# Kernel tuning notes

Hardware: AMD Instinct MI355X
Metric: run time of the kernel (lower is better)

## Reference

```python
import jax, jax.numpy as jnp
import numpy as np

BS, L1, L2, F_IN, HID = 32, 79, 192, 52, 128
E1, E2 = 160, 400            # intra-graph edges per drug / protein graph
SE_IN, SE_HID = L1 * L2, 2000  # 15168, 2000


def _gat(x, src, dst, W, a_s, a_d, b):
    """PyG GATConv, heads=1, add_self_loops=True, negative_slope=0.2; edge_attr ignored (edge_dim=None)."""
    n = x.shape[0]
    h = x @ W                                    # (N, HID)
    loops = jnp.arange(n, dtype=src.dtype)
    s = jnp.concatenate([src, loops])
    d = jnp.concatenate([dst, loops])
    e = jax.nn.leaky_relu((h @ a_s)[s] + (h @ a_d)[d], 0.2)   # (E+N,)
    m = jax.ops.segment_max(e, d, num_segments=n)
    w = jnp.exp(e - m[d])
    denom = jax.ops.segment_sum(w, d, num_segments=n)
    alpha = w / denom[d]                          # segment softmax over incoming edges
    return jax.ops.segment_sum(alpha[:, None] * h[s], d, num_segments=n) + b


def setup_inputs() -> dict:
    key = jax.random.key(0)
    ks = iter(jax.random.split(key, 40))
    def rn(shape, s=0.05):
        return (jax.random.normal(next(ks), shape) * s).astype(jnp.float32)
    rng = np.random.default_rng(0)
    def edges(e_per, n_per):
        off = np.arange(BS)[:, None] * n_per
        src = (rng.integers(0, n_per, (BS, e_per)) + off).reshape(-1)
        dst = (rng.integers(0, n_per, (BS, e_per)) + off).reshape(-1)
        return jnp.asarray(np.stack([src, dst]), dtype=jnp.int32)
    return {
        'x1': rn((BS * L1, F_IN), 1.0),
        'x2': rn((BS * L2, F_IN), 1.0),
        'inter': jax.random.uniform(next(ks), (BS, L1, L2), minval=0.5, maxval=1.5, dtype=jnp.float32),
        'drug_edge_index': edges(E1, L1),
        'prot_edge_index': edges(E2, L2),
        'w1': rn((F_IN, HID)), 'b1': jnp.zeros((HID,), jnp.float32),
        'w2': rn((HID, HID)), 'b2': jnp.zeros((HID,), jnp.float32),
        'gat_w': rn((6, HID, HID)), 'gat_as': rn((6, HID)),
        'gat_ad': rn((6, HID)), 'gat_b': jnp.zeros((6, HID), jnp.float32),
        'se1_w': rn((SE_IN, SE_HID)), 'se1_b': jnp.zeros((SE_HID,), jnp.float32),
        'se2_w': rn((SE_HID, SE_IN)), 'se2_b': jnp.zeros((SE_IN,), jnp.float32),
        'fc1_w': rn((256, 512)), 'fc1_b': jnp.zeros((512,), jnp.float32),
        'fc2_w': rn((512, 256)), 'fc2_b': jnp.zeros((256,), jnp.float32),
        'fc3_w': rn((256, 128)), 'fc3_b': jnp.zeros((128,), jnp.float32),
        'fc4_w': rn((128, 64)), 'fc4_b': jnp.zeros((64,), jnp.float32),
        'out_w': rn((64, 1)), 'out_b': jnp.zeros((1,), jnp.float32),
    }


def reference(x1, x2, inter, drug_edge_index, prot_edge_index,
              w1, b1, w2, b2, gat_w, gat_as, gat_ad, gat_b,
              se1_w, se1_b, se2_w, se2_b,
              fc1_w, fc1_b, fc2_w, fc2_b, fc3_w, fc3_b, fc4_w, fc4_b,
              out_w, out_b):
    relu = jax.nn.relu
    # shared node embedding MLP
    x1 = relu(relu(x1 @ w1 + b1) @ w2 + b2)
    x2 = relu(relu(x2 @ w1 + b1) @ w2 + b2)
    dsrc, ddst = drug_edge_index[0], drug_edge_index[1]
    psrc, pdst = prot_edge_index[0], prot_edge_index[1]
    # drug branch: 3 GAT layers + residual sum
    x11 = relu(_gat(x1, dsrc, ddst, gat_w[0], gat_as[0], gat_ad[0], gat_b[0]))
    x12 = relu(_gat(x11, dsrc, ddst, gat_w[1], gat_as[1], gat_ad[1], gat_b[1]))
    x13 = relu(_gat(x12, dsrc, ddst, gat_w[2], gat_as[2], gat_ad[2], gat_b[2]))
    x_l = (x11 + x12 + x13).reshape(BS, L1, HID)   # to_dense_batch (all graphs same size)
    # protein branch
    x21 = relu(_gat(x2, psrc, pdst, gat_w[3], gat_as[3], gat_ad[3], gat_b[3]))
    x22 = relu(_gat(x21, psrc, pdst, gat_w[4], gat_as[4], gat_ad[4], gat_b[4]))
    x23 = relu(_gat(x22, psrc, pdst, gat_w[5], gat_as[5], gat_ad[5], gat_b[5]))
    x_p = (x21 + x22 + x23).reshape(BS, L2, HID)
    # dense outer-product cross fusion
    inter_att = (1.0 / inter).reshape(BS, SE_IN, 1)
    x_l1 = jnp.repeat(x_l, L2, axis=1)             # (BS, L1*L2, HID)
    x_p1 = jnp.tile(x_p, (1, L1, 1))               # (BS, L1*L2, HID)
    xx = jnp.concatenate([x_l1, x_p1], axis=2)     # (BS, 15168, 256)
    c = xx.mean(axis=2)                            # (BS, 15168)
    c = relu(c @ se1_w + se1_b)
    c = jax.nn.sigmoid(c @ se2_w + se2_b)[:, :, None]
    xx = (xx * c * inter_att).mean(axis=1)         # (BS, 256)
    # head MLP (dropout identity in eval)
    h1 = xx @ fc1_w + fc1_b
    x = relu(h1)
    x = relu(x @ fc2_w + fc2_b)
    x = relu(x @ fc3_w + fc3_b)
    x = relu(x @ fc4_w + fc4_b)
    out = x @ out_w + out_b
    return (out, h1)
```

## Files before the change

kernel.cpp:

```cpp
#include <hip/hip_runtime.h>

#define NDRUG 2528
#define NPROT 6144
#define NTOT  8672
#define EDRUG 5120
#define EPROT 12800
#define ETOT  17920
#define SEIN  15168
#define SEHID 2000
#define NSPLIT 16

__global__ __launch_bounds__(1024) void csr_one(const int* __restrict__ de,
                                                const int* __restrict__ pe,
                                                int* __restrict__ off,
                                                int* __restrict__ eidx) {
    __shared__ int ldeg[NTOT];
    __shared__ int tot[1024];
    const int t = threadIdx.x;
    for (int i = t; i < NTOT; i += 1024) ldeg[i] = 0;
    __syncthreads();
    for (int e = t; e < ETOT; e += 1024) {
        int d;
        if (e < EDRUG) d = de[EDRUG + e];
        else d = pe[EPROT + (e - EDRUG)] + NDRUG;
        atomicAdd(&ldeg[d], 1);
    }
    __syncthreads();
    int loc[9];
    int s = 0;
    const int base = t * 9;
#pragma unroll
    for (int c = 0; c < 9; c++) {
        int idx = base + c;
        int v = (idx < NTOT) ? ldeg[idx] : 0;
        loc[c] = s; s += v;
    }
    tot[t] = s;
    __syncthreads();
    for (int d = 1; d < 1024; d <<= 1) {
        int v = (t >= d) ? tot[t - d] : 0;
        __syncthreads();
        tot[t] += v;
        __syncthreads();
    }
    int pre = (t == 0) ? 0 : tot[t - 1];
#pragma unroll
    for (int c = 0; c < 9; c++) {
        int idx = base + c;
        if (idx < NTOT) { int o = pre + loc[c]; off[idx] = o; ldeg[idx] = o; }
    }
    if (t == 1023) off[NTOT] = tot[1023];
    __syncthreads();
    for (int e = t; e < ETOT; e += 1024) {
        int s2, d;
        if (e < EDRUG) { s2 = de[e]; d = de[EDRUG + e]; }
        else { int ep = e - EDRUG; s2 = pe[ep] + NDRUG; d = pe[EPROT + ep] + NDRUG; }
        int pos = atomicAdd(&ldeg[d], 1);
        eidx[pos] = s2;
    }
}

__global__ void mlp12(const float* __restrict__ x1, const float* __restrict__ x2,
                      const float* __restrict__ w1, const float* __restrict__ b1,
                      const float* __restrict__ w2, const float* __restrict__ b2,
                      float* __restrict__ xA) {
    __shared__ float al[16 * 52];
    __shared__ float hl[16 * 128];
    const int bx = blockIdx.x;
    const int j  = threadIdx.x;
    const int r0 = bx * 16;
    const float* A = (r0 >= NDRUG) ? x2 + (size_t)(r0 - NDRUG) * 52
                                   : x1 + (size_t)r0 * 52;
    for (int idx = j; idx < 16 * 52; idx += 128) al[idx] = A[idx];
    __syncthreads();
    float acc[16];
#pragma unroll
    for (int r = 0; r < 16; r++) acc[r] = 0.f;
    for (int k = 0; k < 52; k++) {
        float bv = w1[k * 128 + j];
#pragma unroll
        for (int r = 0; r < 16; r++) acc[r] += al[r * 52 + k] * bv;
    }
    float bb = b1[j];
#pragma unroll
    for (int r = 0; r < 16; r++) hl[r * 128 + j] = fmaxf(acc[r] + bb, 0.f);
    __syncthreads();
#pragma unroll
    for (int r = 0; r < 16; r++) acc[r] = 0.f;
    for (int k = 0; k < 128; k++) {
        float bv = w2[k * 128 + j];
#pragma unroll
        for (int r = 0; r < 16; r++) acc[r] += hl[r * 128 + k] * bv;
    }
    bb = b2[j];
#pragma unroll
    for (int r = 0; r < 16; r++)
        xA[(size_t)(r0 + r) * 128 + j] = fmaxf(acc[r] + bb, 0.f);
}

__global__ void gat_h2(const float* __restrict__ X, const float* __restrict__ gw,
                       const float* __restrict__ gas, const float* __restrict__ gad,
                       int l, float* __restrict__ H, float* __restrict__ asn,
                       float* __restrict__ adn) {
    __shared__ float al[16 * 128];
    __shared__ float hl[16][129];
    const int bx = blockIdx.x;
    int r0; const float *W, *avs, *avd;
    if (bx < 158) {
        r0 = bx * 16;
        W = gw + (size_t)l * 16384; avs = gas + l * 128; avd = gad + l * 128;
    } else {
        r0 = NDRUG + (bx - 158) * 16;
        W = gw + (size_t)(l + 3) * 16384; avs = gas + (l + 3) * 128; avd = gad + (l + 3) * 128;
    }
    const int j = threadIdx.x;
    for (int idx = j; idx < 16 * 128; idx += 128) al[idx] = X[(size_t)r0 * 128 + idx];
    __syncthreads();
    float acc[16];
#pragma unroll
    for (int r = 0; r < 16; r++) acc[r] = 0.f;
    for (int k = 0; k < 128; k++) {
        float bv = W[k * 128 + j];
#pragma unroll
        for (int r = 0; r < 16; r++) acc[r] += al[r * 128 + k] * bv;
    }
#pragma unroll
    for (int r = 0; r < 16; r++) {
        H[(size_t)(r0 + r) * 128 + j] = acc[r];
        hl[r][j] = acc[r];
    }
    __syncthreads();
    int r = j >> 3, l8 = j & 7;
    float ps = 0.f, pd = 0.f;
    for (int jj = l8; jj < 128; jj += 8) {
        float v = hl[r][jj];
        ps += v * avs[jj];
        pd += v * avd[jj];
    }
    ps += __shfl_down(ps, 4); ps += __shfl_down(ps, 2); ps += __shfl_down(ps, 1);
    pd += __shfl_down(pd, 4); pd += __shfl_down(pd, 2); pd += __shfl_down(pd, 1);
    if (l8 == 0) { asn[r0 + r] = ps; adn[r0 + r] = pd; }
}

__global__ void gat_gather(const int* __restrict__ off, const int* __restrict__ eidx,
                           const float* __restrict__ asn, const float* __restrict__ adn,
                           const float* __restrict__ H, const float* __restrict__ bd,
                           const float* __restrict__ bp, float* __restrict__ Xo,
                           float* __restrict__ xsum, float* __restrict__ sl,
                           int first, int last) {
    __shared__ float sred[4];
    int gid = blockIdx.x * 256 + threadIdx.x;
    int i = gid >> 7, f = gid & 127;
    float adi = adn[i];
    float ev = asn[i] + adi;
    ev = (ev > 0.f) ? ev : 0.2f * ev;
    float w = __expf(ev);
    float acc = w * H[(size_t)i * 128 + f];
    float den = w;
    int e0 = off[i], e1 = off[i + 1];
    for (int e = e0; e < e1; e++) {
        int s = eidx[e];
        float es = asn[s] + adi;
        es = (es > 0.f) ? es : 0.2f * es;
        float we = __expf(es);
        acc += we * H[(size_t)s * 128 + f];
        den += we;
    }
    float bias = (i < NDRUG) ? bd[f] : bp[f];
    float val = fmaxf(acc / den + bias, 0.f);
    if (!last) {
        Xo[gid] = val;
        xsum[gid] = first ? val : (xsum[gid] + val);
    } else {
        float xs = xsum[gid] + val;
        xsum[gid] = xs;
        int t = threadIdx.x;
        float rv = xs;
        rv += __shfl_down(rv, 32); rv += __shfl_down(rv, 16); rv += __shfl_down(rv, 8);
        rv += __shfl_down(rv, 4);  rv += __shfl_down(rv, 2);  rv += __shfl_down(rv, 1);
        if ((t & 63) == 0) sred[t >> 6] = rv;
        __syncthreads();
        if (t == 0) {
            int n0 = blockIdx.x * 2;
            sl[n0]     = sred[0] + sred[1];
            sl[n0 + 1] = sred[2] + sred[3];
        }
    }
}

__global__ void wr1k(const float* __restrict__ W, float* __restrict__ WR1) {
    int k = blockIdx.y * 256 + threadIdx.x;
    int i = blockIdx.x;
    if (k >= SEHID) return;
    const float* p = W + (size_t)(i * 192) * SEHID + k;
    float a0 = 0.f, a1 = 0.f, a2 = 0.f, a3 = 0.f;
    for (int j = 0; j < 192; j += 4) {
        a0 += p[0];
        a1 += p[(size_t)SEHID];
        a2 += p[2 * (size_t)SEHID];
        a3 += p[3 * (size_t)SEHID];
        p += 4 * (size_t)SEHID;
    }
    WR1[i * SEHID + k] = (a0 + a1) + (a2 + a3);
}

__global__ void wc1k(const float* __restrict__ W, float* __restrict__ WC1) {
    int k = blockIdx.y * 256 + threadIdx.x;
    int j = blockIdx.x;
    if (k >= SEHID) return;
    const float* p = W + (size_t)j * SEHID + k;
    const size_t st = (size_t)192 * SEHID;
    float a0 = 0.f, a1 = 0.f, a2 = 0.f, a3 = 0.f;
    int i = 0;
    for (; i < 76; i += 4) {
        a0 += p[0]; a1 += p[st]; a2 += p[2 * st]; a3 += p[3 * st];
        p += 4 * st;
    }
    a0 += p[0]; a1 += p[st]; a2 += p[2 * st];
    WC1[j * SEHID + k] = (a0 + a1) + (a2 + a3);
}

__global__ void se1_small(const float* __restrict__ sl, const float* __restrict__ WR1,
                          const float* __restrict__ WC1, const float* __restrict__ bias,
                          float* __restrict__ cmidT) {
    int k = blockIdx.x * 256 + threadIdx.x;
    int b = blockIdx.y;
    if (k >= SEHID) return;
    float acc = 0.f;
    const float* slr = sl + b * 79;
    for (int i = 0; i < 79; i++)  acc += slr[i] * WR1[i * SEHID + k];
    const float* slp = sl + NDRUG + b * 192;
    for (int j = 0; j < 192; j++) acc += slp[j] * WC1[j * SEHID + k];
    float v = fmaxf(acc * (1.f / 256.f) + bias[k], 0.f);
    cmidT[k * 32 + b] = v;
}

__global__ __launch_bounds__(256) void se2p(const float* __restrict__ cmidT,
                                            const float* __restrict__ W,
                                            float* __restrict__ part) {
    __shared__ float cs[125 * 32];
    const int tid = threadIdx.x;
    const int c0 = blockIdx.x * 512 + tid * 2;
    const int ks = blockIdx.y * 125;
    const float4* csrc = (const float4*)(cmidT + ks * 32);
    for (int idx = tid; idx < 1000; idx += 256)
        ((float4*)cs)[idx] = csrc[idx];
    __syncthreads();
    const bool in = c0 < SEIN;
    float acc0[32], acc1[32];
#pragma unroll
    for (int b = 0; b < 32; b++) { acc0[b] = 0.f; acc1[b] = 0.f; }
    const float2* wp = (const float2*)(W + (size_t)ks * SEIN) + ((in ? c0 : 0) >> 1);
    const size_t wstr = SEIN / 2;
    for (int kk = 0; kk < 125; kk += 25) {
        float2 w[25];
#pragma unroll
        for (int t = 0; t < 25; t++) w[t] = wp[(size_t)t * wstr];
        wp += 25 * wstr;
#pragma unroll
        for (int t = 0; t < 25; t++) {
            const float* cp = cs + (kk + t) * 32;
#pragma unroll
            for (int b4 = 0; b4 < 32; b4 += 4) {
                float4 a = *(const float4*)(cp + b4);
                acc0[b4 + 0] += a.x * w[t].x;  acc1[b4 + 0] += a.x * w[t].y;
                acc0[b4 + 1] += a.y * w[t].x;  acc1[b4 + 1] += a.y * w[t].y;
                acc0[b4 + 2] += a.z * w[t].x;  acc1[b4 + 2] += a.z * w[t].y;
                acc0[b4 + 3] += a.w * w[t].x;  acc1[b4 + 3] += a.w * w[t].y;
            }
        }
    }
    if (in) {
        float* pb = part + (size_t)blockIdx.y * (32 * SEIN) + c0;
#pragma unroll
        for (int b = 0; b < 32; b++) {
            float2 v; v.x = acc0[b]; v.y = acc1[b];
            *(float2*)(pb + (size_t)b * SEIN) = v;
        }
    }
}

__global__ __launch_bounds__(256) void setail(const float* __restrict__ part,
                                              const float* __restrict__ se2b,
                                              const float* __restrict__ inter,
                                              const float* __restrict__ xsum,
                                              float* __restrict__ xx) {
    __shared__ float wl[SEIN];
    __shared__ float wrl[80];
    __shared__ float wcl[192];
    const int b = blockIdx.x, t = threadIdx.x;
    for (int ij = t; ij < SEIN; ij += 256) {
        float s = se2b[ij];
#pragma unroll
        for (int p = 0; p < NSPLIT; p++)
            s += part[(size_t)p * (32 * SEIN) + (size_t)b * SEIN + ij];
        float sig = 1.f / (1.f + __expf(-s));
        wl[ij] = sig / inter[(size_t)b * SEIN + ij];
    }
    __syncthreads();
    if (t < 192) {
        float s = 0.f;
        for (int i = 0; i < 79; i++) s += wl[i * 192 + t];
        wcl[t] = s;
    }
    int wv = t >> 6, ln = t & 63;
    for (int i = wv; i < 79; i += 4) {
        float v = 0.f;
        for (int j = ln; j < 192; j += 64) v += wl[i * 192 + j];
        v += __shfl_down(v, 32); v += __shfl_down(v, 16); v += __shfl_down(v, 8);
        v += __shfl_down(v, 4);  v += __shfl_down(v, 2);  v += __shfl_down(v, 1);
        if (ln == 0) wrl[i] = v;
    }
    __syncthreads();
    float acc = 0.f;
    if (t < 128) {
        for (int i = 0; i < 79; i++)
            acc += xsum[(size_t)(b * 79 + i) * 128 + t] * wrl[i];
    } else {
        int f = t - 128;
        for (int j = 0; j < 192; j++)
            acc += xsum[(size_t)(NDRUG + b * 192 + j) * 128 + f] * wcl[j];
    }
    xx[b * 256 + t] = acc * (1.f / 15168.f);
}

__global__ __launch_bounds__(256) void headk(const float* __restrict__ xx,
                                             const float* __restrict__ fc1w, const float* __restrict__ fc1b,
                                             const float* __restrict__ fc2w, const float* __restrict__ fc2b,
                                             const float* __restrict__ fc3w, const float* __restrict__ fc3b,
                                             const float* __restrict__ fc4w, const float* __restrict__ fc4b,
                                             const float* __restrict__ outw, const float* __restrict__ outb,
                                             float* __restrict__ out) {
    __shared__ float a0[256], a1[512], a2[256], a3[128], a4[64];
    const int b = blockIdx.x, t = threadIdx.x;
    a0[t] = xx[b * 256 + t];
    __syncthreads();
    for (int c = t; c < 512; c += 256) {
        float acc = 0.f;
        for (int k = 0; k < 256; k++) acc += a0[k] * fc1w[(size_t)k * 512 + c];
        float v = acc + fc1b[c];
        out[32 + b * 512 + c] = v;
        a1[c] = fmaxf(v, 0.f);
    }
    __syncthreads();
    {
        float acc = 0.f;
        for (int k = 0; k < 512; k++) acc += a1[k] * fc2w[(size_t)k * 256 + t];
        a2[t] = fmaxf(acc + fc2b[t], 0.f);
    }
    __syncthreads();
    if (t < 128) {
        float acc = 0.f;
        for (int k = 0; k < 256; k++) acc += a2[k] * fc3w[(size_t)k * 128 + t];
        a3[t] = fmaxf(acc + fc3b[t], 0.f);
    }
    __syncthreads();
    if (t < 64) {
        float acc = 0.f;
        for (int k = 0; k < 128; k++) acc += a3[k] * fc4w[(size_t)k * 64 + t];
        a4[t] = fmaxf(acc + fc4b[t], 0.f);
    }
    __syncthreads();
    if (t < 64) {
        float v = a4[t] * outw[t];
        v += __shfl_down(v, 32); v += __shfl_down(v, 16); v += __shfl_down(v, 8);
        v += __shfl_down(v, 4);  v += __shfl_down(v, 2);  v += __shfl_down(v, 1);
        if (t == 0) out[b] = v + outb[0];
    }
}

extern "C" void kernel_launch(void* const* d_in, const int* in_sizes, int n_in,
                              void* d_out, int out_size, void* d_ws, size_t ws_size,
                              hipStream_t stream) {
    const float* x1    = (const float*)d_in[0];
    const float* x2    = (const float*)d_in[1];
    const float* inter = (const float*)d_in[2];
    const int*   de    = (const int*)d_in[3];
    const int*   pe    = (const int*)d_in[4];
    const float* w1    = (const float*)d_in[5];
    const float* b1    = (const float*)d_in[6];
    const float* w2    = (const float*)d_in[7];
    const float* b2    = (const float*)d_in[8];
    const float* gw    = (const float*)d_in[9];
    const float* gas   = (const float*)d_in[10];
    const float* gad   = (const float*)d_in[11];
    const float* gb    = (const float*)d_in[12];
    const float* se1w  = (const float*)d_in[13];
    const float* se1b  = (const float*)d_in[14];
    const float* se2w  = (const float*)d_in[15];
    const float* se2b  = (const float*)d_in[16];
    const float* fc1w  = (const float*)d_in[17];
    const float* fc1b  = (const float*)d_in[18];
    const float* fc2w  = (const float*)d_in[19];
    const float* fc2b  = (const float*)d_in[20];
    const float* fc3w  = (const float*)d_in[21];
    const float* fc3b  = (const float*)d_in[22];
    const float* fc4w  = (const float*)d_in[23];
    const float* fc4b  = (const float*)d_in[24];
    const float* outw  = (const float*)d_in[25];
    const float* outb  = (const float*)d_in[26];
    float* out = (float*)d_out;
    float* ws  = (float*)d_ws;

    const size_t NF = (size_t)NTOT * 128;
    float* xA    = ws;
    float* xB    = xA + NF;
    float* hbuf  = xB + NF;
    float* xsum  = hbuf + NF;
    float* sm    = xsum + NF;
    float* asn   = sm;                     sm += NTOT;
    float* adn   = sm;                     sm += NTOT;
    float* sl    = sm;                     sm += NTOT;
    float* WR1   = sm;                     sm += 79 * SEHID;
    float* WC1   = sm;                     sm += 192 * SEHID;
    float* cmidT = sm;                     sm += 32 * SEHID;
    float* xx    = sm;                     sm += 32 * 256;
    float* part  = sm;                     sm += (size_t)NSPLIT * 32 * SEIN;
    int*   im    = (int*)sm;
    int*   off   = im;                     im += NTOT + 1;
    int*   eidx  = im;                     im += ETOT;

    csr_one<<<1, 1024, 0, stream>>>(de, pe, off, eidx);

    wr1k<<<dim3(79, 8), 256, 0, stream>>>(se1w, WR1);
    wc1k<<<dim3(192, 8), 256, 0, stream>>>(se1w, WC1);

    mlp12<<<542, 128, 0, stream>>>(x1, x2, w1, b1, w2, b2, xA);

    gat_h2<<<542, 128, 0, stream>>>(xA, gw, gas, gad, 0, hbuf, asn, adn);
    gat_gather<<<4336, 256, 0, stream>>>(off, eidx, asn, adn, hbuf,
                                         gb + 0 * 128, gb + 3 * 128,
                                         xB, xsum, sl, 1, 0);
    gat_h2<<<542, 128, 0, stream>>>(xB, gw, gas, gad, 1, hbuf, asn, adn);
    gat_gather<<<4336, 256, 0, stream>>>(off, eidx, asn, adn, hbuf,
                                         gb + 1 * 128, gb + 4 * 128,
                                         xA, xsum, sl, 0, 0);
    gat_h2<<<542, 128, 0, stream>>>(xA, gw, gas, gad, 2, hbuf, asn, adn);
    gat_gather<<<4336, 256, 0, stream>>>(off, eidx, asn, adn, hbuf,
                                         gb + 2 * 128, gb + 5 * 128,
                                         nullptr, xsum, sl, 0, 1);

    se1_small<<<dim3(8, 32), 256, 0, stream>>>(sl, WR1, WC1, se1b, cmidT);
    se2p<<<dim3(30, NSPLIT), 256, 0, stream>>>(cmidT, se2w, part);
    setail<<<32, 256, 0, stream>>>(part, se2b, inter, xsum, xx);

    headk<<<32, 256, 0, stream>>>(xx, fc1w, fc1b, fc2w, fc2b, fc3w, fc3b,
                                  fc4w, fc4b, outw, outb, out);
}
```

Before: 628.0 us.

## Fuse preprocessing kernels, use capped adjacency lists, and restructure SE/tail stages

Replaces the single-block CSR build with a per-node fixed-capacity (64) edge list filled by atomics, and merges it, the first MLP and the WR1 column reduction into one launch. The first GAT projection is merged with the WC1 reduction in a second launch. GAT and MLP matmuls move to 256-thread blocks with float4 shared reads. The SE2 sum and sigmoid run in a separate wide elementwise kernel ahead of a fused tail/head kernel, and the se2p grid is halved. This cuts launch count and removes the serial single-block CSR build. The capped edge list silently drops edges past 64 per node and makes edge order nondeterministic.

```diff
diff --git a/kernel.cpp b/kernel.cpp
--- a/kernel.cpp
+++ b/kernel.cpp
@@ -9,102 +9,107 @@
 #define SEIN  15168
 #define SEHID 2000
 #define NSPLIT 16
-
-__global__ __launch_bounds__(1024) void csr_one(const int* __restrict__ de,
-                                                const int* __restrict__ pe,
-                                                int* __restrict__ off,
-                                                int* __restrict__ eidx) {
-    __shared__ int ldeg[NTOT];
-    __shared__ int tot[1024];
-    const int t = threadIdx.x;
-    for (int i = t; i < NTOT; i += 1024) ldeg[i] = 0;
-    __syncthreads();
-    for (int e = t; e < ETOT; e += 1024) {
-        int d;
-        if (e < EDRUG) d = de[EDRUG + e];
-        else d = pe[EPROT + (e - EDRUG)] + NDRUG;
-        atomicAdd(&ldeg[d], 1);
-    }
-    __syncthreads();
-    int loc[9];
-    int s = 0;
-    const int base = t * 9;
-#pragma unroll
-    for (int c = 0; c < 9; c++) {
-        int idx = base + c;
-        int v = (idx < NTOT) ? ldeg[idx] : 0;
-        loc[c] = s; s += v;
-    }
-    tot[t] = s;
-    __syncthreads();
-    for (int d = 1; d < 1024; d <<= 1) {
-        int v = (t >= d) ? tot[t - d] : 0;
-        __syncthreads();
-        tot[t] += v;
-        __syncthreads();
-    }
-    int pre = (t == 0) ? 0 : tot[t - 1];
-#pragma unroll
-    for (int c = 0; c < 9; c++) {
-        int idx = base + c;
-        if (idx < NTOT) { int o = pre + loc[c]; off[idx] = o; ldeg[idx] = o; }
-    }
-    if (t == 1023) off[NTOT] = tot[1023];
-    __syncthreads();
-    for (int e = t; e < ETOT; e += 1024) {
-        int s2, d;
-        if (e < EDRUG) { s2 = de[e]; d = de[EDRUG + e]; }
-        else { int ep = e - EDRUG; s2 = pe[ep] + NDRUG; d = pe[EPROT + ep] + NDRUG; }
-        int pos = atomicAdd(&ldeg[d], 1);
-        eidx[pos] = s2;
-    }
-}
-
-__global__ void mlp12(const float* __restrict__ x1, const float* __restrict__ x2,
-                      const float* __restrict__ w1, const float* __restrict__ b1,
-                      const float* __restrict__ w2, const float* __restrict__ b2,
-                      float* __restrict__ xA) {
+#define NTOTF (NTOT*128)
+#define ECAP  64
+
+#define FMA4(A, s, W4) { A.x += (s)*(W4).x; A.y += (s)*(W4).y; A.z += (s)*(W4).z; A.w += (s)*(W4).w; }
+
+__global__ __launch_bounds__(256) void k1(const float* __restrict__ x1,
+                                          const float* __restrict__ x2,
+                                          const float* __restrict__ w1,
+                                          const float* __restrict__ b1,
+                                          const float* __restrict__ w2,
+                                          const float* __restrict__ b2,
+                                          float* __restrict__ xA,
+                                          const float* __restrict__ se1w,
+                                          float* __restrict__ WR1,
+                                          const int* __restrict__ de,
+                                          const int* __restrict__ pe,
+                                          int* __restrict__ cnt,
+                                          int* __restrict__ eidxc) {
     __shared__ float al[16 * 52];
     __shared__ float hl[16 * 128];
-    const int bx = blockIdx.x;
-    const int j  = threadIdx.x;
-    const int r0 = bx * 16;
-    const float* A = (r0 >= NDRUG) ? x2 + (size_t)(r0 - NDRUG) * 52
-                                   : x1 + (size_t)r0 * 52;
-    for (int idx = j; idx < 16 * 52; idx += 128) al[idx] = A[idx];
-    __syncthreads();
-    float acc[16];
-#pragma unroll
-    for (int r = 0; r < 16; r++) acc[r] = 0.f;
-    for (int k = 0; k < 52; k++) {
-        float bv = w1[k * 128 + j];
-#pragma unroll
-        for (int r = 0; r < 16; r++) acc[r] += al[r * 52 + k] * bv;
-    }
-    float bb = b1[j];
-#pragma unroll
-    for (int r = 0; r < 16; r++) hl[r * 128 + j] = fmaxf(acc[r] + bb, 0.f);
-    __syncthreads();
-#pragma unroll
-    for (int r = 0; r < 16; r++) acc[r] = 0.f;
-    for (int k = 0; k < 128; k++) {
-        float bv = w2[k * 128 + j];
-#pragma unroll
-        for (int r = 0; r < 16; r++) acc[r] += hl[r * 128 + k] * bv;
-    }
-    bb = b2[j];
-#pragma unroll
-    for (int r = 0; r < 16; r++)
-        xA[(size_t)(r0 + r) * 128 + j] = fmaxf(acc[r] + bb, 0.f);
-}
-
-__global__ void gat_h2(const float* __restrict__ X, const float* __restrict__ gw,
-                       const float* __restrict__ gas, const float* __restrict__ gad,
-                       int l, float* __restrict__ H, float* __restrict__ asn,
-                       float* __restrict__ adn) {
-    __shared__ float al[16 * 128];
-    __shared__ float hl[16][129];
-    const int bx = blockIdx.x;
+    const int bx = blockIdx.x, tid = threadIdx.x;
+    if (bx < 542) {
+        const int u = tid >> 7, j = tid & 127;
+        const int r0 = bx * 16;
+        const float* A = (r0 >= NDRUG) ? x2 + (size_t)(r0 - NDRUG) * 52
+                                       : x1 + (size_t)r0 * 52;
+        for (int idx = tid; idx < 16 * 52; idx += 256) al[idx] = A[idx];
+        __syncthreads();
+        float acc[8];
+#pragma unroll
+        for (int r = 0; r < 8; r++) acc[r] = 0.f;
+        for (int k4 = 0; k4 < 13; k4++) {
+            float c0 = w1[(k4 * 4 + 0) * 128 + j];
+            float c1 = w1[(k4 * 4 + 1) * 128 + j];
+            float c2 = w1[(k4 * 4 + 2) * 128 + j];
+            float c3 = w1[(k4 * 4 + 3) * 128 + j];
+#pragma unroll
+            for (int r = 0; r < 8; r++) {
+                float4 av = ((const float4*)(al + (u * 8 + r) * 52))[k4];
+                acc[r] += av.x * c0 + av.y * c1 + av.z * c2 + av.w * c3;
+            }
+        }
+        float bb = b1[j];
+#pragma unroll
+        for (int r = 0; r < 8; r++) hl[(u * 8 + r) * 128 + j] = fmaxf(acc[r] + bb, 0.f);
+        __syncthreads();
+#pragma unroll
+        for (int r = 0; r < 8; r++) acc[r] = 0.f;
+        for (int k4 = 0; k4 < 32; k4++) {
+            float c0 = w2[(k4 * 4 + 0) * 128 + j];
+            float c1 = w2[(k4 * 4 + 1) * 128 + j];
+            float c2 = w2[(k4 * 4 + 2) * 128 + j];
+            float c3 = w2[(k4 * 4 + 3) * 128 + j];
+#pragma unroll
+            for (int r = 0; r < 8; r++) {
+                float4 av = ((const float4*)(hl + (u * 8 + r) * 128))[k4];
+                acc[r] += av.x * c0 + av.y * c1 + av.z * c2 + av.w * c3;
+            }
+        }
+        bb = b2[j];
+#pragma unroll
+        for (int r = 0; r < 8; r++)
+            xA[(size_t)(r0 + u * 8 + r) * 128 + j] = fmaxf(acc[r] + bb, 0.f);
+    } else if (bx < 700) {
+        int rb = bx - 542;
+        int i = rb >> 1, half = rb & 1;
+        int k4 = half * 256 + tid;
+        if (k4 < 500) {
+            const float4* p = (const float4*)se1w + (size_t)(i * 192) * 500 + k4;
+            float4 acc = {0.f, 0.f, 0.f, 0.f};
+            for (int j0 = 0; j0 < 192; j0 += 8) {
+                float4 v[8];
+#pragma unroll
+                for (int t = 0; t < 8; t++) v[t] = p[(size_t)(j0 + t) * 500];
+#pragma unroll
+                for (int t = 0; t < 8; t++) {
+                    acc.x += v[t].x; acc.y += v[t].y; acc.z += v[t].z; acc.w += v[t].w;
+                }
+            }
+            ((float4*)(WR1 + i * SEHID))[k4] = acc;
+        }
+    } else {
+        int rb = bx - 700;
+        for (int e = rb * 256 + tid; e < ETOT; e += 16 * 256) {
+            int s, d;
+            if (e < EDRUG) { s = de[e]; d = de[EDRUG + e]; }
+            else { int ep = e - EDRUG; s = pe[ep] + NDRUG; d = pe[EPROT + ep] + NDRUG; }
+            int slot = atomicAdd(&cnt[d], 1);
+            if (slot < ECAP) eidxc[(size_t)d * ECAP + slot] = s;
+        }
+    }
+}
+
+__device__ __forceinline__ void gat_h_body(const float* __restrict__ X,
+                                           const float* __restrict__ gw,
+                                           const float* __restrict__ gas,
+                                           const float* __restrict__ gad,
+                                           int l, float* __restrict__ H,
+                                           float* __restrict__ asn, float* __restrict__ adn,
+                                           int bx, int tid, float* al, float* hl) {
+    const int u = tid >> 7, j = tid & 127;
     int r0; const float *W, *avs, *avd;
     if (bx < 158) {
         r0 = bx * 16;
@@ -113,41 +118,107 @@
         r0 = NDRUG + (bx - 158) * 16;
         W = gw + (size_t)(l + 3) * 16384; avs = gas + (l + 3) * 128; avd = gad + (l + 3) * 128;
     }
-    const int j = threadIdx.x;
-    for (int idx = j; idx < 16 * 128; idx += 128) al[idx] = X[(size_t)r0 * 128 + idx];
-    __syncthreads();
-    float acc[16];
-#pragma unroll
-    for (int r = 0; r < 16; r++) acc[r] = 0.f;
-    for (int k = 0; k < 128; k++) {
-        float bv = W[k * 128 + j];
-#pragma unroll
-        for (int r = 0; r < 16; r++) acc[r] += al[r * 128 + k] * bv;
-    }
-#pragma unroll
-    for (int r = 0; r < 16; r++) {
-        H[(size_t)(r0 + r) * 128 + j] = acc[r];
-        hl[r][j] = acc[r];
-    }
-    __syncthreads();
-    int r = j >> 3, l8 = j & 7;
+    for (int idx = tid; idx < 2048; idx += 256) al[idx] = X[(size_t)r0 * 128 + idx];
+    __syncthreads();
+    float acc[8];
+#pragma unroll
+    for (int r = 0; r < 8; r++) acc[r] = 0.f;
+    for (int k4 = 0; k4 < 32; k4++) {
+        float c0 = W[(k4 * 4 + 0) * 128 + j];
+        float c1 = W[(k4 * 4 + 1) * 128 + j];
+        float c2 = W[(k4 * 4 + 2) * 128 + j];
+        float c3 = W[(k4 * 4 + 3) * 128 + j];
+#pragma unroll
+        for (int r = 0; r < 8; r++) {
+            float4 av = ((const float4*)(al + (u * 8 + r) * 128))[k4];
+            acc[r] += av.x * c0 + av.y * c1 + av.z * c2 + av.w * c3;
+        }
+    }
+#pragma unroll
+    for (int r = 0; r < 8; r++) {
+        H[(size_t)(r0 + u * 8 + r) * 128 + j] = acc[r];
+        hl[(u * 8 + r) * 128 + j] = acc[r];
+    }
+    __syncthreads();
+    int rl = j >> 4, l16 = j & 15;
+    int row = u * 8 + rl;
     float ps = 0.f, pd = 0.f;
-    for (int jj = l8; jj < 128; jj += 8) {
-        float v = hl[r][jj];
+    for (int jj = l16; jj < 128; jj += 16) {
+        float v = hl[row * 128 + jj];
         ps += v * avs[jj];
         pd += v * avd[jj];
     }
-    ps += __shfl_down(ps, 4); ps += __shfl_down(ps, 2); ps += __shfl_down(ps, 1);
-    pd += __shfl_down(pd, 4); pd += __shfl_down(pd, 2); pd += __shfl_down(pd, 1);
-    if (l8 == 0) { asn[r0 + r] = ps; adn[r0 + r] = pd; }
-}
-
-__global__ void gat_gather(const int* __restrict__ off, const int* __restrict__ eidx,
-                           const float* __restrict__ asn, const float* __restrict__ adn,
-                           const float* __restrict__ H, const float* __restrict__ bd,
-                           const float* __restrict__ bp, float* __restrict__ Xo,
-                           float* __restrict__ xsum, float* __restrict__ sl,
-                           int first, int last) {
+    ps += __shfl_down(ps, 8, 16); ps += __shfl_down(ps, 4, 16);
+    ps += __shfl_down(ps, 2, 16); ps += __shfl_down(ps, 1, 16);
+    pd += __shfl_down(pd, 8, 16); pd += __shfl_down(pd, 4, 16);
+    pd += __shfl_down(pd, 2, 16); pd += __shfl_down(pd, 1, 16);
+    if (l16 == 0) { asn[r0 + row] = ps; adn[r0 + row] = pd; }
+}
+
+__global__ __launch_bounds__(256) void k2(const float* __restrict__ X,
+                                          const float* __restrict__ gw,
+                                          const float* __restrict__ gas,
+                                          const float* __restrict__ gad,
+                                          float* __restrict__ H,
+                                          float* __restrict__ asn,
+                                          float* __restrict__ adn,
+                                          const float* __restrict__ se1w,
+                                          float* __restrict__ WC1) {
+    __shared__ float al[2048];
+    __shared__ float hl[2048];
+    const int bx = blockIdx.x, tid = threadIdx.x;
+    if (bx < 542) {
+        gat_h_body(X, gw, gas, gad, 0, H, asn, adn, bx, tid, al, hl);
+    } else {
+        int rb = bx - 542;
+        int j = rb >> 1, half = rb & 1;
+        int k4 = half * 256 + tid;
+        if (k4 < 500) {
+            const float4* p = (const float4*)se1w + (size_t)j * 500 + k4;
+            const size_t st = (size_t)192 * 500;
+            float4 acc = {0.f, 0.f, 0.f, 0.f};
+            int i = 0;
+            for (; i + 8 <= 72; i += 8) {
+                float4 v[8];
+#pragma unroll
+                for (int t = 0; t < 8; t++) v[t] = p[(size_t)(i + t) * st];
+#pragma unroll
+                for (int t = 0; t < 8; t++) {
+                    acc.x += v[t].x; acc.y += v[t].y; acc.z += v[t].z; acc.w += v[t].w;
+                }
+            }
+            for (; i < 79; i++) {
+                float4 v = p[(size_t)i * st];
+                acc.x += v.x; acc.y += v.y; acc.z += v.z; acc.w += v.w;
+            }
+            ((float4*)(WC1 + j * SEHID))[k4] = acc;
+        }
+    }
+}
+
+__global__ __launch_bounds__(256) void gath(const float* __restrict__ X,
+                                            const float* __restrict__ gw,
+                                            const float* __restrict__ gas,
+                                            const float* __restrict__ gad,
+                                            int l, float* __restrict__ H,
+                                            float* __restrict__ asn,
+                                            float* __restrict__ adn) {
+    __shared__ float al[2048];
+    __shared__ float hl[2048];
+    gat_h_body(X, gw, gas, gad, l, H, asn, adn, blockIdx.x, threadIdx.x, al, hl);
+}
+
+__global__ __launch_bounds__(256) void gat_gather(const int* __restrict__ cnt,
+                                                  const int* __restrict__ eidxc,
+                                                  const float* __restrict__ asn,
+                                                  const float* __restrict__ adn,
+                                                  const float* __restrict__ H,
+                                                  const float* __restrict__ bd,
+                                                  const float* __restrict__ bp,
+                                                  float* __restrict__ Xo,
+                                                  float* __restrict__ xsum,
+                                                  float* __restrict__ sl,
+                                                  int first, int last) {
     __shared__ float sred[4];
     int gid = blockIdx.x * 256 + threadIdx.x;
     int i = gid >> 7, f = gid & 127;
@@ -157,9 +228,10 @@
     float w = __expf(ev);
     float acc = w * H[(size_t)i * 128 + f];
     float den = w;
-    int e0 = off[i], e1 = off[i + 1];
-    for (int e = e0; e < e1; e++) {
-        int s = eidx[e];
+    int dg = cnt[i]; dg = dg > ECAP ? ECAP : dg;
+    const int* ep = eidxc + (size_t)i * ECAP;
+    for (int e = 0; e < dg; e++) {
+        int s = ep[e];
         float es = asn[s] + adi;
         es = (es > 0.f) ? es : 0.2f * es;
         float we = __expf(es);
@@ -188,41 +260,11 @@
     }
 }
 
-__global__ void wr1k(const float* __restrict__ W, float* __restrict__ WR1) {
-    int k = blockIdx.y * 256 + threadIdx.x;
-    int i = blockIdx.x;
-    if (k >= SEHID) return;
-    const float* p = W + (size_t)(i * 192) * SEHID + k;
-    float a0 = 0.f, a1 = 0.f, a2 = 0.f, a3 = 0.f;
-    for (int j = 0; j < 192; j += 4) {
-        a0 += p[0];
-        a1 += p[(size_t)SEHID];
-        a2 += p[2 * (size_t)SEHID];
-        a3 += p[3 * (size_t)SEHID];
-        p += 4 * (size_t)SEHID;
-    }
-    WR1[i * SEHID + k] = (a0 + a1) + (a2 + a3);
-}
-
-__global__ void wc1k(const float* __restrict__ W, float* __restrict__ WC1) {
-    int k = blockIdx.y * 256 + threadIdx.x;
-    int j = blockIdx.x;
-    if (k >= SEHID) return;
-    const float* p = W + (size_t)j * SEHID + k;
-    const size_t st = (size_t)192 * SEHID;
-    float a0 = 0.f, a1 = 0.f, a2 = 0.f, a3 = 0.f;
-    int i = 0;
-    for (; i < 76; i += 4) {
-        a0 += p[0]; a1 += p[st]; a2 += p[2 * st]; a3 += p[3 * st];
-        p += 4 * st;
-    }
-    a0 += p[0]; a1 += p[st]; a2 += p[2 * st];
-    WC1[j * SEHID + k] = (a0 + a1) + (a2 + a3);
-}
-
-__global__ void se1_small(const float* __restrict__ sl, const float* __restrict__ WR1,
-                          const float* __restrict__ WC1, const float* __restrict__ bias,
-                          float* __restrict__ cmidT) {
+__global__ __launch_bounds__(256) void se1_small(const float* __restrict__ sl,
+                                                 const float* __restrict__ WR1,
+                                                 const float* __restrict__ WC1,
+                                                 const float* __restrict__ bias,
+                                                 float* __restrict__ cmidT) {
     int k = blockIdx.x * 256 + threadIdx.x;
     int b = blockIdx.y;
     if (k >= SEHID) return;
@@ -235,68 +277,93 @@
     cmidT[k * 32 + b] = v;
 }
 
-__global__ __launch_bounds__(256) void se2p(const float* __restrict__ cmidT,
-                                            const float* __restrict__ W,
-                                            float* __restrict__ part) {
-    __shared__ float cs[125 * 32];
+__global__ __launch_bounds__(256, 1) void se2p(const float* __restrict__ cmidT,
+                                               const float* __restrict__ W,
+                                               float* __restrict__ part) {
+    __shared__ float4 cs4[125 * 8];
     const int tid = threadIdx.x;
-    const int c0 = blockIdx.x * 512 + tid * 2;
+    const int c4 = blockIdx.x * 256 + tid;
     const int ks = blockIdx.y * 125;
     const float4* csrc = (const float4*)(cmidT + ks * 32);
-    for (int idx = tid; idx < 1000; idx += 256)
-        ((float4*)cs)[idx] = csrc[idx];
-    __syncthreads();
-    const bool in = c0 < SEIN;
-    float acc0[32], acc1[32];
-#pragma unroll
-    for (int b = 0; b < 32; b++) { acc0[b] = 0.f; acc1[b] = 0.f; }
-    const float2* wp = (const float2*)(W + (size_t)ks * SEIN) + ((in ? c0 : 0) >> 1);
-    const size_t wstr = SEIN / 2;
-    for (int kk = 0; kk < 125; kk += 25) {
-        float2 w[25];
-#pragma unroll
-        for (int t = 0; t < 25; t++) w[t] = wp[(size_t)t * wstr];
-        wp += 25 * wstr;
-#pragma unroll
-        for (int t = 0; t < 25; t++) {
-            const float* cp = cs + (kk + t) * 32;
-#pragma unroll
-            for (int b4 = 0; b4 < 32; b4 += 4) {
-                float4 a = *(const float4*)(cp + b4);
-                acc0[b4 + 0] += a.x * w[t].x;  acc1[b4 + 0] += a.x * w[t].y;
-                acc0[b4 + 1] += a.y * w[t].x;  acc1[b4 + 1] += a.y * w[t].y;
-                acc0[b4 + 2] += a.z * w[t].x;  acc1[b4 + 2] += a.z * w[t].y;
-                acc0[b4 + 3] += a.w * w[t].x;  acc1[b4 + 3] += a.w * w[t].y;
+    for (int idx = tid; idx < 1000; idx += 256) cs4[idx] = csrc[idx];
+    __syncthreads();
+    const bool in = c4 < (SEIN / 4);
+    float4 acc[32];
+#pragma unroll
+    for (int b = 0; b < 32; b++) acc[b] = make_float4(0.f, 0.f, 0.f, 0.f);
+    const float4* wp = (const float4*)W + (size_t)ks * (SEIN / 4) + (in ? c4 : 0);
+    int kk = 0;
+    for (int bt = 0; bt < 12; bt++) {
+        float4 wv[10];
+#pragma unroll
+        for (int t = 0; t < 10; t++) wv[t] = wp[(size_t)t * (SEIN / 4)];
+        wp += (size_t)10 * (SEIN / 4);
+#pragma unroll
+        for (int t = 0; t < 10; t++) {
+            const float4* cp = cs4 + (kk + t) * 8;
+#pragma unroll
+            for (int b8 = 0; b8 < 8; b8++) {
+                float4 a = cp[b8];
+                FMA4(acc[b8 * 4 + 0], a.x, wv[t]);
+                FMA4(acc[b8 * 4 + 1], a.y, wv[t]);
+                FMA4(acc[b8 * 4 + 2], a.z, wv[t]);
+                FMA4(acc[b8 * 4 + 3], a.w, wv[t]);
+            }
+        }
+        kk += 10;
+    }
+    {
+        float4 wv[5];
+#pragma unroll
+        for (int t = 0; t < 5; t++) wv[t] = wp[(size_t)t * (SEIN / 4)];
+#pragma unroll
+        for (int t = 0; t < 5; t++) {
+            const float4* cp = cs4 + (kk + t) * 8;
+#pragma unroll
+            for (int b8 = 0; b8 < 8; b8++) {
+                float4 a = cp[b8];
+                FMA4(acc[b8 * 4 + 0], a.x, wv[t]);
+                FMA4(acc[b8 * 4 + 1], a.y, wv[t]);
+                FMA4(acc[b8 * 4 + 2], a.z, wv[t]);
+                FMA4(acc[b8 * 4 + 3], a.w, wv[t]);
             }
         }
     }
     if (in) {
-        float* pb = part + (size_t)blockIdx.y * (32 * SEIN) + c0;
-#pragma unroll
-        for (int b = 0; b < 32; b++) {
-            float2 v; v.x = acc0[b]; v.y = acc1[b];
-            *(float2*)(pb + (size_t)b * SEIN) = v;
-        }
-    }
-}
-
-__global__ __launch_bounds__(256) void setail(const float* __restrict__ part,
+        float* pb = part + (size_t)blockIdx.y * (32 * SEIN) + (size_t)c4 * 4;
+#pragma unroll
+        for (int b = 0; b < 32; b++)
+            *(float4*)(pb + (size_t)b * SEIN) = acc[b];
+    }
+}
+
+__global__ __launch_bounds__(256) void se2fin(const float* __restrict__ part,
                                               const float* __restrict__ se2b,
                                               const float* __restrict__ inter,
+                                              float* __restrict__ wgt) {
+    int gid = blockIdx.x * 256 + threadIdx.x;
+    int ij = gid % SEIN;
+    float s = se2b[ij];
+#pragma unroll
+    for (int p = 0; p < NSPLIT; p++) s += part[(size_t)p * (32 * SEIN) + gid];
+    float sig = 1.f / (1.f + __expf(-s));
+    wgt[gid] = sig / inter[gid];
+}
+
+__global__ __launch_bounds__(256) void tail32(const float* __restrict__ wgt,
                                               const float* __restrict__ xsum,
-                                              float* __restrict__ xx) {
+                                              const float* __restrict__ fc1w, const float* __restrict__ fc1b,
+                                              const float* __restrict__ fc2w, const float* __restrict__ fc2b,
+                                              const float* __restrict__ fc3w, const float* __restrict__ fc3b,
+                                              const float* __restrict__ fc4w, const float* __restrict__ fc4b,
+                                              const float* __restrict__ outw, const float* __restrict__ outb,
+                                              float* __restrict__ out) {
     __shared__ float wl[SEIN];
-    __shared__ float wrl[80];
-    __shared__ float wcl[192];
+    __shared__ float wrl[79], wcl[192];
+    __shared__ float xxl[256], h1[512], h2[256], h3[128], h4[64];
     const int b = blockIdx.x, t = threadIdx.x;
-    for (int ij = t; ij < SEIN; ij += 256) {
-        float s = se2b[ij];
-#pragma unroll
-        for (int p = 0; p < NSPLIT; p++)
-            s += part[(size_t)p * (32 * SEIN) + (size_t)b * SEIN + ij];
-        float sig = 1.f / (1.f + __expf(-s));
-        wl[ij] = sig / inter[(size_t)b * SEIN + ij];
-    }
+    for (int idx = t; idx < SEIN / 4; idx += 256)
+        ((float4*)wl)[idx] = ((const float4*)(wgt + (size_t)b * SEIN))[idx];
     __syncthreads();
     if (t < 192) {
         float s = 0.f;
@@ -312,57 +379,47 @@
         if (ln == 0) wrl[i] = v;
     }
     __syncthreads();
-    float acc = 0.f;
-    if (t < 128) {
-        for (int i = 0; i < 79; i++)
-            acc += xsum[(size_t)(b * 79 + i) * 128 + t] * wrl[i];
-    } else {
-        int f = t - 128;
-        for (int j = 0; j < 192; j++)
-            acc += xsum[(size_t)(NDRUG + b * 192 + j) * 128 + f] * wcl[j];
-    }
-    xx[b * 256 + t] = acc * (1.f / 15168.f);
-}
-
-__global__ __launch_bounds__(256) void headk(const float* __restrict__ xx,
-                                             const float* __restrict__ fc1w, const float* __restrict__ fc1b,
-                                             const float* __restrict__ fc2w, const float* __restrict__ fc2b,
-                                             const float* __restrict__ fc3w, const float* __restrict__ fc3b,
-                                             const float* __restrict__ fc4w, const float* __restrict__ fc4b,
-                                             const float* __restrict__ outw, const float* __restrict__ outb,
-                                             float* __restrict__ out) {
-    __shared__ float a0[256], a1[512], a2[256], a3[128], a4[64];
-    const int b = blockIdx.x, t = threadIdx.x;
-    a0[t] = xx[b * 256 + t];
+    {
+        float acc = 0.f;
+        if (t < 128) {
+            for (int i = 0; i < 79; i++)
+                acc += xsum[(size_t)(b * 79 + i) * 128 + t] * wrl[i];
+        } else {
+            int f = t - 128;
+            for (int j = 0; j < 192; j++)
+                acc += xsum[(size_t)(NDRUG + b * 192 + j) * 128 + f] * wcl[j];
+        }
+        xxl[t] = acc * (1.f / 15168.f);
+    }
     __syncthreads();
     for (int c = t; c < 512; c += 256) {
         float acc = 0.f;
-        for (int k = 0; k < 256; k++) acc += a0[k] * fc1w[(size_t)k * 512 + c];
+        for (int k = 0; k < 256; k++) acc += xxl[k] * fc1w[(size_t)k * 512 + c];
         float v = acc + fc1b[c];
         out[32 + b * 512 + c] = v;
-        a1[c] = fmaxf(v, 0.f);
+        h1[c] = fmaxf(v, 0.f);
     }
     __syncthreads();
     {
         float acc = 0.f;
-        for (int k = 0; k < 512; k++) acc += a1[k] * fc2w[(size_t)k * 256 + t];
-        a2[t] = fmaxf(acc + fc2b[t], 0.f);
+        for (int k = 0; k < 512; k++) acc += h1[k] * fc2w[(size_t)k * 256 + t];
+        h2[t] = fmaxf(acc + fc2b[t], 0.f);
     }
     __syncthreads();
     if (t < 128) {
         float acc = 0.f;
-        for (int k = 0; k < 256; k++) acc += a2[k] * fc3w[(size_t)k * 128 + t];
-        a3[t] = fmaxf(acc + fc3b[t], 0.f);
+        for (int k = 0; k < 256; k++) acc += h2[k] * fc3w[(size_t)k * 128 + t];
+        h3[t] = fmaxf(acc + fc3b[t], 0.f);
     }
     __syncthreads();
     if (t < 64) {
         float acc = 0.f;
-        for (int k = 0; k < 128; k++) acc += a3[k] * fc4w[(size_t)k * 64 + t];
-        a4[t] = fmaxf(acc + fc4b[t], 0.f);
+        for (int k = 0; k < 128; k++) acc += h3[k] * fc4w[(size_t)k * 64 + t];
+        h4[t] = fmaxf(acc + fc4b[t], 0.f);
     }
     __syncthreads();
     if (t < 64) {
-        float v = a4[t] * outw[t];
+        float v = h4[t] * outw[t];
         v += __shfl_down(v, 32); v += __shfl_down(v, 16); v += __shfl_down(v, 8);
         v += __shfl_down(v, 4);  v += __shfl_down(v, 2);  v += __shfl_down(v, 1);
         if (t == 0) out[b] = v + outb[0];
@@ -414,36 +471,32 @@
     float* WR1   = sm;                     sm += 79 * SEHID;
     float* WC1   = sm;                     sm += 192 * SEHID;
     float* cmidT = sm;                     sm += 32 * SEHID;
-    float* xx    = sm;                     sm += 32 * 256;
+    float* wgt   = sm;                     sm += 32 * SEIN;
     float* part  = sm;                     sm += (size_t)NSPLIT * 32 * SEIN;
-    int*   im    = (int*)sm;
-    int*   off   = im;                     im += NTOT + 1;
-    int*   eidx  = im;                     im += ETOT;
-
-    csr_one<<<1, 1024, 0, stream>>>(de, pe, off, eidx);
-
-    wr1k<<<dim3(79, 8), 256, 0, stream>>>(se1w, WR1);
-    wc1k<<<dim3(192, 8), 256, 0, stream>>>(se1w, WC1);
-
-    mlp12<<<542, 128, 0, stream>>>(x1, x2, w1, b1, w2, b2, xA);
-
-    gat_h2<<<542, 128, 0, stream>>>(xA, gw, gas, gad, 0, hbuf, asn, adn);
-    gat_gather<<<4336, 256, 0, stream>>>(off, eidx, asn, adn, hbuf,
+    int*   cnt   = (int*)sm;
+    int*   eidxc = cnt + NTOT;
+
+    hipMemsetAsync(cnt, 0, NTOT * sizeof(int), stream);
+
+    k1<<<716, 256, 0, stream>>>(x1, x2, w1, b1, w2, b2, xA, se1w, WR1, de, pe, cnt, eidxc);
+
+    k2<<<926, 256, 0, stream>>>(xA, gw, gas, gad, hbuf, asn, adn, se1w, WC1);
+
+    gat_gather<<<4336, 256, 0, stream>>>(cnt, eidxc, asn, adn, hbuf,
                                          gb + 0 * 128, gb + 3 * 128,
                                          xB, xsum, sl, 1, 0);
-    gat_h2<<<542, 128, 0, stream>>>(xB, gw, gas, gad, 1, hbuf, asn, adn);
-    gat_gather<<<4336, 256, 0, stream>>>(off, eidx, asn, adn, hbuf,
+    gath<<<542, 256, 0, stream>>>(xB, gw, gas, gad, 1, hbuf, asn, adn);
+    gat_gather<<<4336, 256, 0, stream>>>(cnt, eidxc, asn, adn, hbuf,
                                          gb + 1 * 128, gb + 4 * 128,
                                          xA, xsum, sl, 0, 0);
-    gat_h2<<<542, 128, 0, stream>>>(xA, gw, gas, gad, 2, hbuf, asn, adn);
-    gat_gather<<<4336, 256, 0, stream>>>(off, eidx, asn, adn, hbuf,
+    gath<<<542, 256, 0, stream>>>(xA, gw, gas, gad, 2, hbuf, asn, adn);
+    gat_gather<<<4336, 256, 0, stream>>>(cnt, eidxc, asn, adn, hbuf,
                                          gb + 2 * 128, gb + 5 * 128,
                                          nullptr, xsum, sl, 0, 1);
 
     se1_small<<<dim3(8, 32), 256, 0, stream>>>(sl, WR1, WC1, se1b, cmidT);
-    se2p<<<dim3(30, NSPLIT), 256, 0, stream>>>(cmidT, se2w, part);
-    setail<<<32, 256, 0, stream>>>(part, se2b, inter, xsum, xx);
-
-    headk<<<32, 256, 0, stream>>>(xx, fc1w, fc1b, fc2w, fc2b, fc3w, fc3b,
-                                  fc4w, fc4b, outw, outb, out);
-}
+    se2p<<<dim3(15, NSPLIT), 256, 0, stream>>>(cmidT, se2w, part);
+    se2fin<<<1896, 256, 0, stream>>>(part, se2b, inter, wgt);
+    tail32<<<32, 256, 0, stream>>>(wgt, xsum, fc1w, fc1b, fc2w, fc2b,
+                                   fc3w, fc3b, fc4w, fc4b, outw, outb, out);
+}
```

Result: faster. 505.3 us (-19.5%).
